# Performance work log

Hardware: AMD Instinct MI355X
Metric: run time of the kernel (lower is better)

## Reference

```python
import jax, jax.numpy as jnp
import numpy as np

B, T, E = 2, 2048, 1024
H = 16
D = E // H  # head_dim = 64


def setup_inputs() -> dict:
    key = jax.random.key(0)
    ks = jax.random.split(key, 9)
    s = 1.0 / np.sqrt(E)
    inp = {"x": jax.random.normal(ks[0], (B, T, E), dtype=jnp.float32)}
    # Linear params (torch nn.Linear: y = x @ W.T + b)
    inp["Wq"] = jax.random.uniform(ks[1], (E, E), jnp.float32, -s, s)
    inp["bq"] = jax.random.uniform(ks[2], (E,), jnp.float32, -s, s)
    inp["Wk"] = jax.random.uniform(ks[3], (E, E), jnp.float32, -s, s)
    inp["bk"] = jax.random.uniform(ks[4], (E,), jnp.float32, -s, s)
    inp["Wv"] = jax.random.uniform(ks[5], (E, E), jnp.float32, -s, s)
    inp["bv"] = jax.random.uniform(ks[6], (E,), jnp.float32, -s, s)
    inp["Wo"] = jax.random.uniform(ks[7], (E, E), jnp.float32, -s, s)
    inp["bo"] = jax.random.uniform(ks[8], (E,), jnp.float32, -s, s)
    return inp


def reference(x, Wq, bq, Wk, bk, Wv, bv, Wo, bo):
    # QKV projections, reshape to [B, H, T, D]
    def split_heads(y):
        return y.reshape(B, T, H, D).transpose(0, 2, 1, 3)

    Q = split_heads(x @ Wq.T + bq)
    K = split_heads(x @ Wk.T + bk)
    V = split_heads(x @ Wv.T + bv)

    scale = 1.0 / jnp.sqrt(jnp.asarray(D, x.dtype))
    scores = jnp.einsum("bhqd,bhkd->bhqk", Q, K) * scale  # [B,H,T,T]
    attn = jax.nn.softmax(scores, axis=-1)
    out = jnp.einsum("bhqk,bhkd->bhqd", attn, V)  # [B,H,T,D]
    out = out.transpose(0, 2, 1, 3).reshape(B, T, E)
    # dropout is identity in eval mode
    return out @ Wo.T + bo
```

## Files before the change

### kernel.cpp

```cpp
#include <hip/hip_runtime.h>
#include <math.h>

#define BB 2
#define TT 2048
#define EE 1024
#define HH 16
#define DD 64
#define MM (BB*TT)
#define KK EE

typedef short bf16x8 __attribute__((ext_vector_type(8)));
typedef float f32x4  __attribute__((ext_vector_type(4)));

__device__ __forceinline__ unsigned short f2bf(float f) {
  unsigned int u = __float_as_uint(f);
  u = (u + 0x7FFFu + ((u >> 16) & 1u)) >> 16;
  return (unsigned short)u;
}

__device__ __forceinline__ void async16(const void* g, void* l) {
  __builtin_amdgcn_global_load_lds(
      (const __attribute__((address_space(1))) unsigned int*)g,
      (__attribute__((address_space(3))) unsigned int*)l, 16, 0, 0);
}

__global__ __launch_bounds__(256) void to_bf16(
    const float* __restrict__ x,  const float* __restrict__ wq,
    const float* __restrict__ wk, const float* __restrict__ wv,
    const float* __restrict__ wo,
    unsigned short* __restrict__ xh, unsigned short* __restrict__ wcat,
    unsigned short* __restrict__ woh)
{
  int c = blockIdx.x * 256 + threadIdx.x;
  const float* src; unsigned short* dst; int off;
  if (c < 1048576) { src = x; dst = xh; off = c; }
  else {
    int r = c - 1048576;
    int w = r >> 18;
    off = r & 262143;
    if      (w == 0) { src = wq; dst = wcat; }
    else if (w == 1) { src = wk; dst = wcat + (1 << 20); }
    else if (w == 2) { src = wv; dst = wcat + (2 << 20); }
    else             { src = wo; dst = woh; }
  }
  float4 v = ((const float4*)src)[off];
  ushort4 h;
  h.x = f2bf(v.x); h.y = f2bf(v.y); h.z = f2bf(v.z); h.w = f2bf(v.w);
  ((ushort4*)dst)[off] = h;
}

template<int MODE>
__global__ __launch_bounds__(512) void gemm_bf16(
    const unsigned short* __restrict__ A, const unsigned short* __restrict__ B,
    const float* __restrict__ b0p, const float* __restrict__ b1p,
    const float* __restrict__ b2p,
    unsigned short* __restrict__ oq, unsigned short* __restrict__ ok,
    unsigned short* __restrict__ ov, float* __restrict__ ofp, float qscale)
{
  constexpr int NT = (MODE == 0) ? 128 : 64;
  constexpr int JN = NT / 32;
  constexpr int BROWS = NT * 32;
  constexpr int TOT = (MODE == 0) ? 16 : 12;
  __shared__ unsigned short S[(MODE == 0) ? 17408 : 12288];

  const int tid  = threadIdx.x;
  const int lane = tid & 63;
  const int wv   = tid >> 6;
  const int col  = lane & 15;
  const int quad = lane >> 4;
  const int wm = (wv & 3) * 32;
  const int wn = (wv >> 2) * (NT / 2);
  const int m0 = blockIdx.x * 128;
  const int n0 = blockIdx.y * NT;

  const int srow = lane >> 2;
  const int sw16 = (((lane & 3) ^ ((lane >> 2) & 3)) << 3);
  const int fswA = ((quad ^ (col & 3)) << 3);

  auto stage = [&](int kt, int b) {
#pragma unroll
    for (int s = 0; s < 2; ++s) {
      const int t = wv * 2 + s;
      if (t < TOT) {
        const unsigned short* src; int rb, g0, loff;
        if (t < 8) { src = A; rb = t * 16;       g0 = m0; loff = b * 4096; }
        else       { src = B; rb = (t - 8) * 16; g0 = n0; loff = 8192 + b * BROWS; }
        async16(src + (size_t)(g0 + rb + srow) * KK + kt + sw16,
                S + loff + rb * 32);
      }
    }
  };

  f32x4 acc[2][JN];
  const f32x4 z = {0.f, 0.f, 0.f, 0.f};
#pragma unroll
  for (int i = 0; i < 2; ++i)
#pragma unroll
    for (int j = 0; j < JN; ++j) acc[i][j] = z;

  stage(0, 0);
  __syncthreads();

  for (int kt = 0; kt < KK; kt += 32) {
    const int buf = (kt >> 5) & 1;
    if (kt + 32 < KK) stage(kt + 32, buf ^ 1);

    const unsigned short* Asb = S + buf * 4096;
    const unsigned short* Bsb = S + 8192 + buf * BROWS;
    bf16x8 bf[JN];
#pragma unroll
    for (int j = 0; j < JN; ++j)
      bf[j] = *(const bf16x8*)(Bsb + (wn + j * 16 + col) * 32 + fswA);
#pragma unroll
    for (int i = 0; i < 2; ++i) {
      bf16x8 af = *(const bf16x8*)(Asb + (wm + i * 16 + col) * 32 + fswA);
#pragma unroll
      for (int j = 0; j < JN; ++j)
        acc[i][j] = __builtin_amdgcn_mfma_f32_16x16x32_bf16(af, bf[j], acc[i][j], 0, 0, 0);
    }
    __syncthreads();
  }

  unsigned short* Cs = S;
  if (MODE == 0) {
    const int region = n0 >> 10;
    const float* bias = (region == 0) ? b0p : (region == 1) ? b1p : b2p;
    const float scl = (region == 0) ? qscale : 1.0f;
    const int nlbase = n0 & 1023;
    const int h0 = nlbase >> 6;
    const int b = m0 >> 11, t0 = m0 & (TT - 1);
    if (region < 2) {
#pragma unroll
      for (int i = 0; i < 2; ++i)
#pragma unroll
        for (int j = 0; j < 4; ++j) {
          const int nt = wn + j * 16 + col;
          const float bs = bias[nlbase + nt];
#pragma unroll
          for (int r = 0; r < 4; ++r) {
            const int mt = wm + i * 16 + quad * 4 + r;
            Cs[mt * 136 + nt] = f2bf((acc[i][j][r] + bs) * scl);
          }
        }
      __syncthreads();
      unsigned short* dst = (region == 0) ? oq : ok;
#pragma unroll
      for (int s = 0; s < 4; ++s) {
        const int u = s * 512 + tid;
        const int mt = u >> 4, hs = (u >> 3) & 1, ch = u & 7;
        const size_t g = ((size_t)(b * HH + h0 + hs) * TT + t0 + mt) * DD + ch * 8;
        *(uint4*)(dst + g) = *(const uint4*)(Cs + mt * 136 + hs * 64 + ch * 8);
      }
    } else {
#pragma unroll
      for (int i = 0; i < 2; ++i)
#pragma unroll
        for (int j = 0; j < 4; ++j) {
          const int nt = wn + j * 16 + col;
          const float bs = bias[nlbase + nt];
          ushort4 pk;
          pk.x = f2bf(acc[i][j][0] + bs);
          pk.y = f2bf(acc[i][j][1] + bs);
          pk.z = f2bf(acc[i][j][2] + bs);
          pk.w = f2bf(acc[i][j][3] + bs);
          *(ushort4*)(Cs + nt * 136 + wm + i * 16 + quad * 4) = pk;
        }
      __syncthreads();
#pragma unroll
      for (int s = 0; s < 4; ++s) {
        const int u = s * 512 + tid;
        const int nt = u >> 4, ch = u & 15;
        const int d = nt & 63, hs = nt >> 6;
        const size_t g = ((size_t)(b * HH + h0 + hs) * DD + d) * TT + t0 + ch * 8;
        *(uint4*)(ov + g) = *(const uint4*)(Cs + nt * 136 + ch * 8);
      }
    }
  } else {
#pragma unroll
    for (int i = 0; i < 2; ++i) {
#pragma unroll
      for (int j = 0; j < JN; ++j) {
        const int n = n0 + wn + j * 16 + col;
        const float bs = b0p[n];
#pragma unroll
        for (int r = 0; r < 4; ++r) {
          const int m = m0 + wm + i * 16 + quad * 4 + r;
          ofp[(size_t)m * EE + n] = acc[i][j][r] + bs;
        }
      }
    }
  }
}

__global__ __launch_bounds__(512) void flash_mfma(
    const unsigned short* __restrict__ Qb, const unsigned short* __restrict__ Kb,
    const unsigned short* __restrict__ Vtb, unsigned short* __restrict__ ctx)
{
  __shared__ unsigned short QPs[128 * 72];
  __shared__ unsigned short Ks[2][64 * 64];
  __shared__ unsigned short Vts[2][64 * 64];

  const int tid  = threadIdx.x;
  const int lane = tid & 63;
  const int wv   = tid >> 6;
  const int col  = lane & 15;
  const int quad = lane >> 4;
  const int wm   = wv * 16;
  const int gid  = blockIdx.x;
  const int bh   = gid & 31;
  const int q0   = (gid >> 5) * 128;

  const unsigned short* Qg = Qb  + (size_t)bh * TT * DD;
  const unsigned short* Kg = Kb  + (size_t)bh * TT * DD;
  const unsigned short* Vg = Vtb + (size_t)bh * DD * TT;

  const int srow = lane >> 3;
  const int sw16 = (((lane & 7) ^ ((lane >> 3) & 7)) << 3);
  const int cxor = (col & 7);

  auto stage_kv = [&](int kt, int b) {
#pragma unroll
    for (int s = 0; s < 2; ++s) {
      const int rb = (wv & 3) * 16 + s * 8;
      if (wv < 4)
        async16(Kg + (size_t)(kt + rb + srow) * DD + sw16, &Ks[b][rb * 64]);
      else
        async16(Vg + (size_t)(rb + srow) * TT + kt + sw16, &Vts[b][rb * 64]);
    }
  };

#pragma unroll
  for (int s = 0; s < 2; ++s) {
    const int rb = wv * 16 + s * 8;
    async16(Qg + (size_t)(q0 + rb + srow) * DD + sw16, &QPs[rb * 64]);
  }
  stage_kv(0, 0);
  __syncthreads();

  bf16x8 aq[2];
#pragma unroll
  for (int h = 0; h < 2; ++h)
    aq[h] = *(const bf16x8*)(QPs + (wm + col) * 64 +
                             (((h * 4 + quad) ^ cxor) << 3));
  __syncthreads();

  f32x4 o_acc[4];
  float lpart = 0.f;
  const f32x4 z = {0.f, 0.f, 0.f, 0.f};
#pragma unroll
  for (int j = 0; j < 4; ++j) o_acc[j] = z;

  for (int kt = 0; kt < TT; kt += 64) {
    const int buf = (kt >> 6) & 1;
    if (kt + 64 < TT) stage_kv(kt + 64, buf ^ 1);

    f32x4 sacc[4];
#pragma unroll
    for (int j = 0; j < 4; ++j) sacc[j] = z;

#pragma unroll
    for (int j = 0; j < 4; ++j) {
      bf16x8 bk0 = *(const bf16x8*)(Ks[buf] + (j * 16 + col) * 64 + ((quad ^ cxor) << 3));
      bf16x8 bk1 = *(const bf16x8*)(Ks[buf] + (j * 16 + col) * 64 + (((4 + quad) ^ cxor) << 3));
      sacc[j] = __builtin_amdgcn_mfma_f32_16x16x32_bf16(bk0, aq[0], sacc[j], 0, 0, 0);
      sacc[j] = __builtin_amdgcn_mfma_f32_16x16x32_bf16(bk1, aq[1], sacc[j], 0, 0, 0);
    }

    {
      const int prow = (wm + col) * 72;
      float lp = 0.f;
#pragma unroll
      for (int j = 0; j < 4; ++j) {
        float p0 = __builtin_amdgcn_exp2f(sacc[j][0]);
        float p1 = __builtin_amdgcn_exp2f(sacc[j][1]);
        float p2 = __builtin_amdgcn_exp2f(sacc[j][2]);
        float p3 = __builtin_amdgcn_exp2f(sacc[j][3]);
        lp += (p0 + p1) + (p2 + p3);
        uint2 w;
        w.x = __builtin_amdgcn_perm(__float_as_uint(p1), __float_as_uint(p0), 0x07060302u);
        w.y = __builtin_amdgcn_perm(__float_as_uint(p3), __float_as_uint(p2), 0x07060302u);
        *(uint2*)(QPs + prow + j * 16 + quad * 4) = w;
      }
      lpart += lp;
    }

    bf16x8 ap0 = *(const bf16x8*)(QPs + (wm + col) * 72 + quad * 8);
    bf16x8 ap1 = *(const bf16x8*)(QPs + (wm + col) * 72 + 32 + quad * 8);

#pragma unroll
    for (int j = 0; j < 4; ++j) {
      bf16x8 bv0 = *(const bf16x8*)(Vts[buf] + (j * 16 + col) * 64 + ((quad ^ cxor) << 3));
      bf16x8 bv1 = *(const bf16x8*)(Vts[buf] + (j * 16 + col) * 64 + (((4 + quad) ^ cxor) << 3));
      o_acc[j] = __builtin_amdgcn_mfma_f32_16x16x32_bf16(ap0, bv0, o_acc[j], 0, 0, 0);
      o_acc[j] = __builtin_amdgcn_mfma_f32_16x16x32_bf16(ap1, bv1, o_acc[j], 0, 0, 0);
    }

    __syncthreads();
  }

  unsigned short* Cs = &Ks[0][0];
  const int b = bh >> 4, h = bh & 15;
  float l = lpart;
  l += __shfl_xor(l, 16);
  l += __shfl_xor(l, 32);
#pragma unroll
  for (int r = 0; r < 4; ++r) {
    const float inv = 1.0f / __shfl(l, quad * 4 + r);
    const int trow = wm + quad * 4 + r;
#pragma unroll
    for (int j = 0; j < 4; ++j) {
      const int n = j * 16 + col;
      const int ch = ((n >> 3) ^ (trow & 7)) << 3;
      Cs[trow * 64 + ch + (n & 7)] = f2bf(o_acc[j][r] * inv);
    }
  }
  __syncthreads();
#pragma unroll
  for (int s = 0; s < 2; ++s) {
    const int u = s * 512 + tid;
    const int mr = u >> 3, ch = u & 7;
    const size_t g = ((size_t)(b * TT + q0 + mr)) * EE + h * DD + ch * 8;
    const int chs = (ch ^ (mr & 7)) << 3;
    *(uint4*)(ctx + g) = *(const uint4*)(Cs + mr * 64 + chs);
  }
}

extern "C" void kernel_launch(void* const* d_in, const int* in_sizes, int n_in,
                              void* d_out, int out_size, void* d_ws, size_t ws_size,
                              hipStream_t stream) {
  const float* x  = (const float*)d_in[0];
  const float* Wq = (const float*)d_in[1];
  const float* bq = (const float*)d_in[2];
  const float* Wk = (const float*)d_in[3];
  const float* bk = (const float*)d_in[4];
  const float* Wv = (const float*)d_in[5];
  const float* bv = (const float*)d_in[6];
  const float* Wo = (const float*)d_in[7];
  const float* bo = (const float*)d_in[8];

  unsigned short* p = (unsigned short*)d_ws;
  const size_t XN = (size_t)MM * EE;
  const size_t WN = (size_t)EE * EE;
  unsigned short* x_h    = p;           p += XN;
  unsigned short* Wcat_h = p;           p += 3 * WN;
  unsigned short* Wo_h   = p;           p += WN;
  unsigned short* Qb     = p;           p += XN;
  unsigned short* Kb     = p;           p += XN;
  unsigned short* Vtb    = p;           p += XN;
  unsigned short* ctx_h  = x_h;

  to_bf16<<<8192, 256, 0, stream>>>(x, Wq, Wk, Wv, Wo, x_h, Wcat_h, Wo_h);

  const float qscale = 0.125f * 1.44269504088896f;

  gemm_bf16<0><<<dim3(MM / 128, 3 * EE / 128), 512, 0, stream>>>(
      x_h, Wcat_h, bq, bk, bv, Qb, Kb, Vtb, nullptr, qscale);

  flash_mfma<<<dim3((TT / 128) * BB * HH), 512, 0, stream>>>(Qb, Kb, Vtb, ctx_h);

  gemm_bf16<2><<<dim3(MM / 128, EE / 64), 512, 0, stream>>>(
      ctx_h, Wo_h, bo, nullptr, nullptr,
      nullptr, nullptr, nullptr, (float*)d_out, 1.0f);
}
```

Before: 193.3 us.

## Split attention over two key halves with atomic fp32 accumulation and normalize pass

The flash attention kernel now launches twice as many blocks, each handling half of the key sequence. Each block adds its unnormalized fp32 output and row sums into global buffers with atomics, after the buffers are zeroed with memsets. A new kernel then divides by the row sums and writes the bf16 context in head-interleaved layout. The aim is more parallelism and more blocks per CU, paid for with extra global traffic, atomics, two memsets and an extra kernel launch.

```diff
diff --git a/kernel.cpp b/kernel.cpp
--- a/kernel.cpp
+++ b/kernel.cpp
@@ -194,7 +194,8 @@
 
 __global__ __launch_bounds__(512) void flash_mfma(
     const unsigned short* __restrict__ Qb, const unsigned short* __restrict__ Kb,
-    const unsigned short* __restrict__ Vtb, unsigned short* __restrict__ ctx)
+    const unsigned short* __restrict__ Vtb, float* __restrict__ og,
+    float* __restrict__ lg)
 {
   __shared__ unsigned short QPs[128 * 72];
   __shared__ unsigned short Ks[2][64 * 64];
@@ -208,7 +209,9 @@
   const int wm   = wv * 16;
   const int gid  = blockIdx.x;
   const int bh   = gid & 31;
-  const int q0   = (gid >> 5) * 128;
+  const int half = (gid >> 5) & 1;
+  const int q0   = (gid >> 6) * 128;
+  const int k0   = half << 10;
 
   const unsigned short* Qg = Qb  + (size_t)bh * TT * DD;
   const unsigned short* Kg = Kb  + (size_t)bh * TT * DD;
@@ -234,7 +237,7 @@
     const int rb = wv * 16 + s * 8;
     async16(Qg + (size_t)(q0 + rb + srow) * DD + sw16, &QPs[rb * 64]);
   }
-  stage_kv(0, 0);
+  stage_kv(k0, 0);
   __syncthreads();
 
   bf16x8 aq[2];
@@ -244,15 +247,15 @@
                              (((h * 4 + quad) ^ cxor) << 3));
   __syncthreads();
 
-  f32x4 o_acc[4];
+  f32x4 oacc[4];
   float lpart = 0.f;
   const f32x4 z = {0.f, 0.f, 0.f, 0.f};
 #pragma unroll
-  for (int j = 0; j < 4; ++j) o_acc[j] = z;
-
-  for (int kt = 0; kt < TT; kt += 64) {
+  for (int j = 0; j < 4; ++j) oacc[j] = z;
+
+  for (int kt = k0; kt < k0 + 1024; kt += 64) {
     const int buf = (kt >> 6) & 1;
-    if (kt + 64 < TT) stage_kv(kt + 64, buf ^ 1);
+    if (kt + 64 < k0 + 1024) stage_kv(kt + 64, buf ^ 1);
 
     f32x4 sacc[4];
 #pragma unroll
@@ -291,38 +294,44 @@
     for (int j = 0; j < 4; ++j) {
       bf16x8 bv0 = *(const bf16x8*)(Vts[buf] + (j * 16 + col) * 64 + ((quad ^ cxor) << 3));
       bf16x8 bv1 = *(const bf16x8*)(Vts[buf] + (j * 16 + col) * 64 + (((4 + quad) ^ cxor) << 3));
-      o_acc[j] = __builtin_amdgcn_mfma_f32_16x16x32_bf16(ap0, bv0, o_acc[j], 0, 0, 0);
-      o_acc[j] = __builtin_amdgcn_mfma_f32_16x16x32_bf16(ap1, bv1, o_acc[j], 0, 0, 0);
+      oacc[j] = __builtin_amdgcn_mfma_f32_16x16x32_bf16(ap0, bv0, oacc[j], 0, 0, 0);
+      oacc[j] = __builtin_amdgcn_mfma_f32_16x16x32_bf16(ap1, bv1, oacc[j], 0, 0, 0);
     }
 
     __syncthreads();
   }
 
-  unsigned short* Cs = &Ks[0][0];
-  const int b = bh >> 4, h = bh & 15;
   float l = lpart;
   l += __shfl_xor(l, 16);
   l += __shfl_xor(l, 32);
+  if (quad == 0)
+    atomicAdd(lg + (size_t)bh * TT + q0 + wm + col, l);
+  float* ob = og + (size_t)bh * TT * DD + (size_t)(q0 + wm) * DD;
 #pragma unroll
   for (int r = 0; r < 4; ++r) {
-    const float inv = 1.0f / __shfl(l, quad * 4 + r);
-    const int trow = wm + quad * 4 + r;
-#pragma unroll
-    for (int j = 0; j < 4; ++j) {
-      const int n = j * 16 + col;
-      const int ch = ((n >> 3) ^ (trow & 7)) << 3;
-      Cs[trow * 64 + ch + (n & 7)] = f2bf(o_acc[j][r] * inv);
-    }
-  }
-  __syncthreads();
-#pragma unroll
-  for (int s = 0; s < 2; ++s) {
-    const int u = s * 512 + tid;
-    const int mr = u >> 3, ch = u & 7;
-    const size_t g = ((size_t)(b * TT + q0 + mr)) * EE + h * DD + ch * 8;
-    const int chs = (ch ^ (mr & 7)) << 3;
-    *(uint4*)(ctx + g) = *(const uint4*)(Cs + mr * 64 + chs);
-  }
+    const int trow = quad * 4 + r;
+#pragma unroll
+    for (int j = 0; j < 4; ++j)
+      atomicAdd(ob + trow * DD + j * 16 + col, oacc[j][r]);
+  }
+}
+
+__global__ __launch_bounds__(256) void normalize_ctx(
+    const float* __restrict__ o, const float* __restrict__ l,
+    unsigned short* __restrict__ ctx)
+{
+  const int idx = blockIdx.x * 256 + threadIdx.x;
+  const int bh = idx >> 15;
+  const int rem = idx & 32767;
+  const int t = rem >> 4;
+  const int dc = (rem & 15) * 4;
+  float4 v = ((const float4*)o)[idx];
+  const float inv = 1.0f / l[(size_t)bh * TT + t];
+  ushort4 h;
+  h.x = f2bf(v.x * inv); h.y = f2bf(v.y * inv);
+  h.z = f2bf(v.z * inv); h.w = f2bf(v.w * inv);
+  const int b = bh >> 4, hh = bh & 15;
+  *(ushort4*)(ctx + ((size_t)(b * TT + t)) * EE + hh * DD + dc) = h;
 }
 
 extern "C" void kernel_launch(void* const* d_in, const int* in_sizes, int n_in,
@@ -347,7 +356,9 @@
   unsigned short* Qb     = p;           p += XN;
   unsigned short* Kb     = p;           p += XN;
   unsigned short* Vtb    = p;           p += XN;
-  unsigned short* ctx_h  = x_h;
+  float* o_acc = (float*)p;             p += 2 * XN;
+  unsigned short* ctx_h = x_h;
+  float* l_buf = (float*)Wcat_h;
 
   to_bf16<<<8192, 256, 0, stream>>>(x, Wq, Wk, Wv, Wo, x_h, Wcat_h, Wo_h);
 
@@ -356,7 +367,13 @@
   gemm_bf16<0><<<dim3(MM / 128, 3 * EE / 128), 512, 0, stream>>>(
       x_h, Wcat_h, bq, bk, bv, Qb, Kb, Vtb, nullptr, qscale);
 
-  flash_mfma<<<dim3((TT / 128) * BB * HH), 512, 0, stream>>>(Qb, Kb, Vtb, ctx_h);
+  hipMemsetAsync(o_acc, 0, (size_t)BB * HH * TT * DD * sizeof(float), stream);
+  hipMemsetAsync(l_buf, 0, (size_t)BB * HH * TT * sizeof(float), stream);
+
+  flash_mfma<<<dim3((TT / 128) * BB * HH * 2), 512, 0, stream>>>(
+      Qb, Kb, Vtb, o_acc, l_buf);
+
+  normalize_ctx<<<4096, 256, 0, stream>>>(o_acc, l_buf, ctx_h);
 
   gemm_bf16<2><<<dim3(MM / 128, EE / 64), 512, 0, stream>>>(
       ctx_h, Wo_h, bo, nullptr, nullptr,
```

New measurement: 212.7 us. 1.1x slower.
